# Kernel optimization log

Measured on AMD Instinct MI355X. Metric: run time of the kernel, lower is better.

## Reference

```python
import jax, jax.numpy as jnp
import numpy as np

NEG_SLOPE = 0.2  # PyG GATv2 default LeakyReLU slope

N_NODES, N_EDGES, DIMS, HEADS = 50000, 800000, 32, 6
D = DIMS * HEADS  # 192


def setup_inputs() -> dict:
    key = jax.random.key(0)
    ks = jax.random.split(key, 6)
    scale = 1.0 / np.sqrt(D)
    x = jax.random.normal(ks[0], (N_NODES, D), dtype=jnp.float32)
    W_l = jax.random.normal(ks[1], (D, D), dtype=jnp.float32) * scale
    b_l = jnp.zeros((D,), dtype=jnp.float32)
    W_r = jax.random.normal(ks[2], (D, D), dtype=jnp.float32) * scale
    b_r = jnp.zeros((D,), dtype=jnp.float32)
    att = jax.random.normal(ks[3], (HEADS, DIMS), dtype=jnp.float32) * scale
    bias = jnp.zeros((D,), dtype=jnp.float32)
    edge_index = jax.random.randint(ks[4], (2, N_EDGES), 0, N_NODES, dtype=jnp.int64)
    return {"x": x, "W_l": W_l, "b_l": b_l, "W_r": W_r, "b_r": b_r,
            "att": att, "bias": bias, "edge_index": edge_index}


def reference(x, W_l, b_l, W_r, b_r, att, bias, edge_index):
    N = x.shape[0]
    H, C = att.shape
    # linear projections (GATv2: separate source/target transforms)
    x_l = (x @ W_l.T + b_l).reshape(N, H, C)  # source-side
    x_r = (x @ W_r.T + b_r).reshape(N, H, C)  # target-side
    # add self loops (PyG default add_self_loops=True)
    loops = jnp.arange(N, dtype=edge_index.dtype)
    src = jnp.concatenate([edge_index[0], loops])
    dst = jnp.concatenate([edge_index[1], loops])
    # GATv2 attention: e = att . leaky_relu(x_l[src] + x_r[dst])
    m = x_l[src] + x_r[dst]                                   # [E, H, C]
    score = jnp.sum(jax.nn.leaky_relu(m, NEG_SLOPE) * att, -1)  # [E, H]
    # segment softmax over incoming edges of each dst node
    smax = jax.ops.segment_max(score, dst, num_segments=N)     # [N, H]
    ex = jnp.exp(score - smax[dst])
    denom = jax.ops.segment_sum(ex, dst, num_segments=N)
    alpha = ex / (denom[dst] + 1e-16)                          # [E, H]
    # weighted aggregation of source features
    out = jax.ops.segment_sum(alpha[..., None] * x_l[src], dst, num_segments=N)
    out = out.reshape(N, H * C) + bias
    # ResLayer (first=False): residual + ReLU; dropout is identity in eval
    return jax.nn.relu(x + out)
```

## Files before the change

### kernel.cpp

```cpp
#include <hip/hip_runtime.h>

#define DD 192
#define MAXD 96

typedef float f32x4 __attribute__((ext_vector_type(4)));
typedef unsigned int u32x4 __attribute__((ext_vector_type(4)));
typedef __fp16 h2 __attribute__((ext_vector_type(2)));
typedef __fp16 h8 __attribute__((ext_vector_type(8)));

static inline int ceil_div(int a, int b){ return (a + b - 1) / b; }
static inline size_t alignup(size_t x){ return (x + 511) & ~(size_t)511; }

static __device__ __forceinline__ h2 as_h2(unsigned u){ union{unsigned i; h2 h;} c; c.i=u; return c.h; }
static __device__ __forceinline__ unsigned as_u(h2 h){ union{h2 h; unsigned i;} c; c.h=h; return c.i; }

#define DPPA(p, ctrl) do { \
    int _t = __builtin_amdgcn_update_dpp(0, __float_as_int(p), ctrl, 0xf, 0xf, true); \
    (p) += __int_as_float(_t); } while (0)
#define RED8(p)  do { DPPA(p,0xB1); DPPA(p,0x4E); DPPA(p,0x141); } while (0)

__global__ __launch_bounds__(256) void k1_conv_zero(
    const float* __restrict__ Wl, const float* __restrict__ Wr,
    __fp16* __restrict__ wcomb, int* __restrict__ deg, int N, int convB)
{
    const int b = blockIdx.x, t = threadIdx.x;
    if (b < convB) {
        int i = b * 256 + t;
        if (i >= DD * DD) return;
        int row = i / DD, k = i - row * DD;
        int j = row >> 4, r = row & 15;
        int sw = (r & 7) << 3;
        size_t base = (size_t)j * 6144;
        wcomb[base + ((      r * 192 + k) ^ sw)] = (__fp16)Wl[i];
        wcomb[base + (((16 + r) * 192 + k) ^ sw)] = (__fp16)Wr[i];
    } else {
        int i = (b - convB) * 256 + t;
        if (i < N) deg[i] = 0;
    }
}

__global__ __launch_bounds__(256) void k2_proj_scatter(
    const float* __restrict__ x, const __fp16* __restrict__ wcomb,
    const float* __restrict__ bl, const float* __restrict__ br,
    __fp16* __restrict__ xlh, __fp16* __restrict__ xrh, int N,
    const int* __restrict__ ei, int* __restrict__ deg, int* __restrict__ colp,
    int E, int projB)
{
    __shared__ __fp16 wbuf[2][6144];
    const int t = threadIdx.x;

    if ((int)blockIdx.x >= projB) {
        int e0 = (((int)blockIdx.x - projB) * 256 + t) * 2;
        if (e0 < E) {
            int2 s2 = *(const int2*)(ei + e0);
            int2 d2 = *(const int2*)(ei + E + e0);
            int p0 = atomicAdd(&deg[d2.x], 1);
            if (p0 < MAXD - 1) colp[d2.x * MAXD + p0] = s2.x;
            int p1 = atomicAdd(&deg[d2.y], 1);
            if (p1 < MAXD - 1) colp[d2.y * MAXD + p1] = s2.y;
        }
        return;
    }

    const int lane = t & 63;
    int n0 = blockIdx.x * 64 + (t >> 6) * 16;
    if (n0 > N - 16) n0 = N - 16;
    const int rr = lane & 15;
    const int kg = lane >> 4;
    const int sw = (rr & 7) << 3;

    const u32x4* wsrc = (const u32x4*)wcomb;

    u32x4 st[3];
    #pragma unroll
    for (int q = 0; q < 3; ++q) st[q] = wsrc[q * 256 + t];

    h8 ah[6];
    const float* xrow = x + (size_t)(n0 + rr) * DD + kg * 8;
    #pragma unroll
    for (int s = 0; s < 6; ++s) {
        f32x4 v0 = *(const f32x4*)(xrow + 32 * s);
        f32x4 v1 = *(const f32x4*)(xrow + 32 * s + 4);
        union { h2 p[4]; h8 v; } u;
        u.p[0] = __builtin_amdgcn_cvt_pkrtz(v0[0], v0[1]);
        u.p[1] = __builtin_amdgcn_cvt_pkrtz(v0[2], v0[3]);
        u.p[2] = __builtin_amdgcn_cvt_pkrtz(v1[0], v1[1]);
        u.p[3] = __builtin_amdgcn_cvt_pkrtz(v1[2], v1[3]);
        ah[s] = u.v;
    }

    #pragma unroll
    for (int q = 0; q < 3; ++q) ((u32x4*)wbuf[0])[q * 256 + t] = st[q];
    __syncthreads();

    #pragma unroll 1
    for (int j = 0; j < 12; ++j) {
        const int cb = j & 1;
        if (j < 11) {
            #pragma unroll
            for (int q = 0; q < 3; ++q)
                st[q] = wsrc[(size_t)(j + 1) * 768 + q * 256 + t];
        }

        f32x4 aL = {0.f, 0.f, 0.f, 0.f};
        f32x4 aR = {0.f, 0.f, 0.f, 0.f};
        const __fp16* wb = wbuf[cb];
        #pragma unroll
        for (int s = 0; s < 6; ++s) {
            const int ko = kg * 8 + 32 * s;
            h8 bL = *(const h8*)&wb[( rr       * 192 + ko) ^ sw];
            h8 bR = *(const h8*)&wb[((16 + rr) * 192 + ko) ^ sw];
            aL = __builtin_amdgcn_mfma_f32_16x16x32_f16(ah[s], bL, aL, 0, 0, 0);
            aR = __builtin_amdgcn_mfma_f32_16x16x32_f16(ah[s], bR, aR, 0, 0, 0);
        }

        if (j < 11) {
            #pragma unroll
            for (int q = 0; q < 3; ++q) ((u32x4*)wbuf[cb ^ 1])[q * 256 + t] = st[q];
        }

        const int col = 16 * j + rr;
        const float bcl = bl[col], bcr = br[col];
        #pragma unroll
        for (int r = 0; r < 4; ++r) {
            size_t o = (size_t)(n0 + kg * 4 + r) * DD + col;
            xlh[o] = (__fp16)(aL[r] + bcl);
            xrh[o] = (__fp16)(aR[r] + bcr);
        }
        __syncthreads();
    }
}

__global__ __launch_bounds__(256) void agg_kernel(
    const __fp16* __restrict__ xlh, const __fp16* __restrict__ xrh,
    const float* __restrict__ att,
    const float* __restrict__ x, const float* __restrict__ bias,
    const int* __restrict__ deg, const int* __restrict__ colp,
    float* __restrict__ out, int N)
{
    const int node = blockIdx.x * 4 + (threadIdx.x >> 6);
    if (node >= N) return;
    const int lane = threadIdx.x & 63;
    const int l16  = lane & 15;
    const int q    = lane >> 4;
    const float LOG2E = 1.4426950408889634f;

    h2 xr_[3][2], w6[3][2], w4[3][2];
    {
        const char* pr = (const char*)xrh + (size_t)node * 384 + 8 * l16;
        #pragma unroll
        for (int s = 0; s < 3; ++s) {
            uint2 u = *(const uint2*)(pr + 128 * s);
            xr_[s][0] = as_h2(u.x);
            xr_[s][1] = as_h2(u.y);
            f32x4 wv = *(const f32x4*)(att + 64 * s + 4 * l16);
            w6[s][0] = __builtin_amdgcn_cvt_pkrtz(0.6f * LOG2E * wv[0], 0.6f * LOG2E * wv[1]);
            w6[s][1] = __builtin_amdgcn_cvt_pkrtz(0.6f * LOG2E * wv[2], 0.6f * LOG2E * wv[3]);
            w4[s][0] = __builtin_amdgcn_cvt_pkrtz(0.4f * LOG2E * wv[0], 0.4f * LOG2E * wv[1]);
            w4[s][1] = __builtin_amdgcn_cvt_pkrtz(0.4f * LOG2E * wv[2], 0.4f * LOG2E * wv[3]);
        }
    }

    float acc[3][4] = {{0.f,0.f,0.f,0.f},{0.f,0.f,0.f,0.f},{0.f,0.f,0.f,0.f}};
    float den[3] = {0.f, 0.f, 0.f};

    const int dg    = min(deg[node], MAXD - 1);
    const int total = dg + 1;
    const int base  = node * MAXD;

    auto srcat = [&](int slot) -> int {
        bool v = slot < total;
        int cidx = base + ((v && slot > 0) ? slot - 1 : 0);
        int cv = colp[cidx];
        return (slot == 0 || !v) ? node : cv;
    };

    uint2 cur0, cur1, cur2, nxt0, nxt1, nxt2;
    {
        const char* pc = (const char*)xlh + (size_t)srcat(q) * 384 + 8 * l16;
        cur0 = *(const uint2*)(pc);
        cur1 = *(const uint2*)(pc + 128);
        cur2 = *(const uint2*)(pc + 256);
    }
    int s_nxt = srcat(4 + q);

    for (int i = 0; i < total; i += 4) {
        int s_n2 = srcat(i + 8 + q);
        const char* pn = (const char*)xlh + (size_t)s_nxt * 384 + 8 * l16;
        nxt0 = *(const uint2*)(pn);
        nxt1 = *(const uint2*)(pn + 128);
        nxt2 = *(const uint2*)(pn + 256);

        const bool vc = (i + q) < total;
        #pragma unroll
        for (int s = 0; s < 3; ++s) {
            const uint2 cu = (s == 0) ? cur0 : (s == 1) ? cur1 : cur2;
            h2 a0 = as_h2(cu.x), a1 = as_h2(cu.y);
            h2 u0 = a0 + xr_[s][0], u1 = a1 + xr_[s][1];
            h2 b0 = as_h2(as_u(u0) & 0x7FFF7FFFu);
            h2 b1 = as_h2(as_u(u1) & 0x7FFF7FFFu);
            float p = __builtin_amdgcn_fdot2(u0, w6[s][0], 0.f, false);
            p = __builtin_amdgcn_fdot2(b0, w4[s][0], p, false);
            p = __builtin_amdgcn_fdot2(u1, w6[s][1], p, false);
            p = __builtin_amdgcn_fdot2(b1, w4[s][1], p, false);
            RED8(p);
            p = vc ? p : -1e30f;
            float e = exp2f(p);
            den[s] += e;
            acc[s][0] = fmaf((float)a0.x, e, acc[s][0]);
            acc[s][1] = fmaf((float)a0.y, e, acc[s][1]);
            acc[s][2] = fmaf((float)a1.x, e, acc[s][2]);
            acc[s][3] = fmaf((float)a1.y, e, acc[s][3]);
        }
        cur0 = nxt0; cur1 = nxt1; cur2 = nxt2;
        s_nxt = s_n2;
    }

    #pragma unroll
    for (int s = 0; s < 3; ++s) {
        den[s] += __shfl_xor(den[s], 16); den[s] += __shfl_xor(den[s], 32);
        #pragma unroll
        for (int j = 0; j < 4; ++j) {
            acc[s][j] += __shfl_xor(acc[s][j], 16);
            acc[s][j] += __shfl_xor(acc[s][j], 32);
        }
    }

    if (q == 0) {
        #pragma unroll
        for (int s = 0; s < 3; ++s) {
            float inv = __builtin_amdgcn_rcpf(den[s] + 1e-16f);
            f32x4 xv = *(const f32x4*)(x + (size_t)node * DD + 64 * s + 4 * l16);
            f32x4 bv = *(const f32x4*)(bias + 64 * s + 4 * l16);
            f32x4 o;
            #pragma unroll
            for (int j = 0; j < 4; ++j) {
                float v = fmaf(acc[s][j], inv, xv[j] + bv[j]);
                o[j] = v > 0.f ? v : 0.f;
            }
            *(f32x4*)(out + (size_t)node * DD + 64 * s + 4 * l16) = o;
        }
    }
}

extern "C" void kernel_launch(void* const* d_in, const int* in_sizes, int n_in,
                              void* d_out, int out_size, void* d_ws, size_t ws_size,
                              hipStream_t stream)
{
    const float* x    = (const float*)d_in[0];
    const float* Wl   = (const float*)d_in[1];
    const float* bl   = (const float*)d_in[2];
    const float* Wr   = (const float*)d_in[3];
    const float* br   = (const float*)d_in[4];
    const float* att  = (const float*)d_in[5];
    const float* bias = (const float*)d_in[6];
    const int*   ei   = (const int*)d_in[7];

    const int N = in_sizes[0] / DD;
    const int E = in_sizes[7] / 2;
    const int convB = ceil_div(DD * DD, 256);
    const int zeroB = ceil_div(N, 256);
    const int edgeB = ceil_div(E, 512);
    const int projB = ceil_div(N, 64);

    float* out = (float*)d_out;
    char*  ws  = (char*)d_ws;

    size_t off = 0;
    __fp16* xlh = (__fp16*)(ws + off); off = alignup(off + (size_t)N * DD * 2);
    __fp16* xrh = (__fp16*)(ws + off); off = alignup(off + (size_t)N * DD * 2);
    __fp16* wcomb = (__fp16*)(ws + off); off = alignup(off + (size_t)12 * 6144 * 2);
    int* deg  = (int*)(ws + off); off = alignup(off + (size_t)N * 4);
    int* colp = (int*)(ws + off); off = alignup(off + (size_t)N * MAXD * 4);

    k1_conv_zero<<<convB + zeroB, 256, 0, stream>>>(Wl, Wr, wcomb, deg, N, convB);
    k2_proj_scatter<<<projB + edgeB, 256, 0, stream>>>(x, wcomb, bl, br, xlh, xrh, N,
                                                       ei, deg, colp, E, projB);
    agg_kernel<<<ceil_div(N, 4), 256, 0, stream>>>(xlh, xrh, att, x, bias, deg, colp, out, N);
}
```

Baseline: 119.0 us.

## Widen projection blocks to 512 threads, stage weights in two halves, prescale column offsets

The projection kernel now uses 512-thread blocks covering 128 nodes. It loads half of the combined weight matrix (six column tiles) into a larger shared buffer at once, instead of double-buffering one tile per iteration with a barrier each step. This cuts barriers per block from twelve to a few and amortizes weight loads over more nodes, at the cost of 72KB shared memory and more registers, which lowers occupancy. Separately, the edge scatter stores byte offsets (source*384) in the adjacency list, so the aggregation kernel skips a multiply and 64-bit index math per neighbor.

```diff
diff --git a/kernel.cpp b/kernel.cpp
--- a/kernel.cpp
+++ b/kernel.cpp
@@ -39,31 +39,31 @@
     }
 }
 
-__global__ __launch_bounds__(256) void k2_proj_scatter(
+__global__ __launch_bounds__(512) void k2_proj_scatter(
     const float* __restrict__ x, const __fp16* __restrict__ wcomb,
     const float* __restrict__ bl, const float* __restrict__ br,
     __fp16* __restrict__ xlh, __fp16* __restrict__ xrh, int N,
     const int* __restrict__ ei, int* __restrict__ deg, int* __restrict__ colp,
     int E, int projB)
 {
-    __shared__ __fp16 wbuf[2][6144];
+    __shared__ __fp16 wbuf[36864];
     const int t = threadIdx.x;
 
     if ((int)blockIdx.x >= projB) {
-        int e0 = (((int)blockIdx.x - projB) * 256 + t) * 2;
+        int e0 = (((int)blockIdx.x - projB) * 512 + t) * 2;
         if (e0 < E) {
             int2 s2 = *(const int2*)(ei + e0);
             int2 d2 = *(const int2*)(ei + E + e0);
             int p0 = atomicAdd(&deg[d2.x], 1);
-            if (p0 < MAXD - 1) colp[d2.x * MAXD + p0] = s2.x;
+            if (p0 < MAXD - 1) colp[d2.x * MAXD + p0] = s2.x * 384;
             int p1 = atomicAdd(&deg[d2.y], 1);
-            if (p1 < MAXD - 1) colp[d2.y * MAXD + p1] = s2.y;
+            if (p1 < MAXD - 1) colp[d2.y * MAXD + p1] = s2.y * 384;
         }
         return;
     }
 
     const int lane = t & 63;
-    int n0 = blockIdx.x * 64 + (t >> 6) * 16;
+    int n0 = blockIdx.x * 128 + (t >> 6) * 16;
     if (n0 > N - 16) n0 = N - 16;
     const int rr = lane & 15;
     const int kg = lane >> 4;
@@ -71,9 +71,9 @@
 
     const u32x4* wsrc = (const u32x4*)wcomb;
 
-    u32x4 st[3];
-    #pragma unroll
-    for (int q = 0; q < 3; ++q) st[q] = wsrc[q * 256 + t];
+    u32x4 st[9];
+    #pragma unroll
+    for (int q = 0; q < 9; ++q) st[q] = wsrc[q * 512 + t];
 
     h8 ah[6];
     const float* xrow = x + (size_t)(n0 + rr) * DD + kg * 8;
@@ -90,21 +90,15 @@
     }
 
     #pragma unroll
-    for (int q = 0; q < 3; ++q) ((u32x4*)wbuf[0])[q * 256 + t] = st[q];
+    for (int q = 0; q < 9; ++q) ((u32x4*)wbuf)[q * 512 + t] = st[q];
     __syncthreads();
 
-    #pragma unroll 1
-    for (int j = 0; j < 12; ++j) {
-        const int cb = j & 1;
-        if (j < 11) {
-            #pragma unroll
-            for (int q = 0; q < 3; ++q)
-                st[q] = wsrc[(size_t)(j + 1) * 768 + q * 256 + t];
-        }
-
+    #pragma unroll
+    for (int q = 0; q < 9; ++q) st[q] = wsrc[4608 + q * 512 + t];
+
+    auto tile = [&](int j, const __fp16* wb) {
         f32x4 aL = {0.f, 0.f, 0.f, 0.f};
         f32x4 aR = {0.f, 0.f, 0.f, 0.f};
-        const __fp16* wb = wbuf[cb];
         #pragma unroll
         for (int s = 0; s < 6; ++s) {
             const int ko = kg * 8 + 32 * s;
@@ -113,12 +107,6 @@
             aL = __builtin_amdgcn_mfma_f32_16x16x32_f16(ah[s], bL, aL, 0, 0, 0);
             aR = __builtin_amdgcn_mfma_f32_16x16x32_f16(ah[s], bR, aR, 0, 0, 0);
         }
-
-        if (j < 11) {
-            #pragma unroll
-            for (int q = 0; q < 3; ++q) ((u32x4*)wbuf[cb ^ 1])[q * 256 + t] = st[q];
-        }
-
         const int col = 16 * j + rr;
         const float bcl = bl[col], bcr = br[col];
         #pragma unroll
@@ -127,8 +115,18 @@
             xlh[o] = (__fp16)(aL[r] + bcl);
             xrh[o] = (__fp16)(aR[r] + bcr);
         }
-        __syncthreads();
-    }
+    };
+
+    #pragma unroll
+    for (int jj = 0; jj < 6; ++jj) tile(jj, wbuf + jj * 6144);
+
+    __syncthreads();
+    #pragma unroll
+    for (int q = 0; q < 9; ++q) ((u32x4*)wbuf)[q * 512 + t] = st[q];
+    __syncthreads();
+
+    #pragma unroll
+    for (int jj = 0; jj < 6; ++jj) tile(jj + 6, wbuf + jj * 6144);
 }
 
 __global__ __launch_bounds__(256) void agg_kernel(
@@ -167,17 +165,18 @@
     const int dg    = min(deg[node], MAXD - 1);
     const int total = dg + 1;
     const int base  = node * MAXD;
+    const int self_off = node * 384;
 
     auto srcat = [&](int slot) -> int {
         bool v = slot < total;
         int cidx = base + ((v && slot > 0) ? slot - 1 : 0);
         int cv = colp[cidx];
-        return (slot == 0 || !v) ? node : cv;
+        return (slot == 0 || !v) ? self_off : cv;
     };
 
     uint2 cur0, cur1, cur2, nxt0, nxt1, nxt2;
     {
-        const char* pc = (const char*)xlh + (size_t)srcat(q) * 384 + 8 * l16;
+        const char* pc = (const char*)xlh + srcat(q) + 8 * l16;
         cur0 = *(const uint2*)(pc);
         cur1 = *(const uint2*)(pc + 128);
         cur2 = *(const uint2*)(pc + 256);
@@ -186,7 +185,7 @@
 
     for (int i = 0; i < total; i += 4) {
         int s_n2 = srcat(i + 8 + q);
-        const char* pn = (const char*)xlh + (size_t)s_nxt * 384 + 8 * l16;
+        const char* pn = (const char*)xlh + s_nxt + 8 * l16;
         nxt0 = *(const uint2*)(pn);
         nxt1 = *(const uint2*)(pn + 128);
         nxt2 = *(const uint2*)(pn + 256);
@@ -260,8 +259,8 @@
     const int E = in_sizes[7] / 2;
     const int convB = ceil_div(DD * DD, 256);
     const int zeroB = ceil_div(N, 256);
-    const int edgeB = ceil_div(E, 512);
-    const int projB = ceil_div(N, 64);
+    const int edgeB = ceil_div(E, 1024);
+    const int projB = ceil_div(N, 128);
 
     float* out = (float*)d_out;
     char*  ws  = (char*)d_ws;
@@ -274,7 +273,7 @@
     int* colp = (int*)(ws + off); off = alignup(off + (size_t)N * MAXD * 4);
 
     k1_conv_zero<<<convB + zeroB, 256, 0, stream>>>(Wl, Wr, wcomb, deg, N, convB);
-    k2_proj_scatter<<<projB + edgeB, 256, 0, stream>>>(x, wcomb, bl, br, xlh, xrh, N,
+    k2_proj_scatter<<<projB + edgeB, 512, 0, stream>>>(x, wcomb, bl, br, xlh, xrh, N,
                                                        ei, deg, colp, E, projB);
     agg_kernel<<<ceil_div(N, 4), 256, 0, stream>>>(xlh, xrh, att, x, bias, deg, colp, out, N);
 }
```

New measurement: 131.8 us. 1.11x slower.
